# Performance work log

Measured on AMD Instinct MI355X. Metric: run time of the kernel, lower is better.

The kernel has to match this reference:

```python
import jax, jax.numpy as jnp
import numpy as np

B, L, D, H = 2, 2048, 1024, 16
DK = D // H
DFF = 4 * D
EPS = 1e-5  # torch LayerNorm default


def setup_inputs() -> dict:
    key = jax.random.key(0)
    ks = jax.random.split(key, 12)
    w = lambda k, shp: (jax.random.normal(k, shp, jnp.float32) * 0.02)
    return {
        "x": jax.random.normal(ks[0], (B, L, D), jnp.float32),
        "y": jax.random.normal(ks[1], (B, L, D), jnp.float32),
        "Wq": w(ks[2], (D, D)), "bq": jnp.zeros((D,), jnp.float32),
        "Wk": w(ks[3], (D, D)), "bk": jnp.zeros((D,), jnp.float32),
        "Wv": w(ks[4], (D, D)), "bv": jnp.zeros((D,), jnp.float32),
        "Wo": w(ks[5], (D, D)), "bo": jnp.zeros((D,), jnp.float32),
        "W1": w(ks[6], (D, DFF)), "b1": jnp.zeros((DFF,), jnp.float32),
        "W2": w(ks[7], (DFF, D)), "b2": jnp.zeros((D,), jnp.float32),
        "ln1_w": jnp.ones((L, D), jnp.float32), "ln1_b": jnp.zeros((L, D), jnp.float32),
        "ln2_w": jnp.ones((L, D), jnp.float32), "ln2_b": jnp.zeros((L, D), jnp.float32),
    }


def _layernorm2d(t, w, b):
    # nn.LayerNorm(normalized_shape=[L, D]): normalize jointly over last two dims
    mu = jnp.mean(t, axis=(-2, -1), keepdims=True)
    var = jnp.mean((t - mu) ** 2, axis=(-2, -1), keepdims=True)
    return (t - mu) * jax.lax.rsqrt(var + EPS) * w + b


def _attention(q_in, kv_in, Wq, bq, Wk, bk, Wv, bv, Wo, bo):
    split = lambda t: t.reshape(B, L, H, DK).transpose(0, 2, 1, 3)  # [B,H,L,DK]
    q = split(q_in @ Wq + bq)
    k = split(kv_in @ Wk + bk)
    v = split(kv_in @ Wv + bv)
    scores = jnp.einsum("bhqd,bhkd->bhqk", q, k) / (DK ** 0.5)
    # NOTE: original applies torch.tril to SCORES (zeroes upper triangle,
    # NOT -inf), so future positions still contribute exp(0)=1 in softmax.
    scores = jnp.tril(scores)
    p_attn = jax.nn.softmax(scores, axis=-1)
    out = jnp.einsum("bhqk,bhkd->bhqd", p_attn, v)
    out = out.transpose(0, 2, 1, 3).reshape(B, L, D)
    return out @ Wo + bo


def reference(x, y, Wq, bq, Wk, bk, Wv, bv, Wo, bo, W1, b1, W2, b2,
              ln1_w, ln1_b, ln2_w, ln2_b):
    # sublayer 0: pre-norm y, attention(query=x, key=value=norm(y)), residual
    y1 = y + _attention(x, _layernorm2d(y, ln1_w, ln1_b),
                        Wq, bq, Wk, bk, Wv, bv, Wo, bo)
    # sublayer 1: pre-norm, FFN (dropout inactive in eval), residual
    h = jax.nn.relu(_layernorm2d(y1, ln2_w, ln2_b) @ W1 + b1)
    return y1 + h @ W2 + b2
```

## Files before the change

kernel.cpp:

```cpp
#include <hip/hip_runtime.h>
#include <math.h>

#define B 2
#define L 2048
#define D 1024
#define H 16
#define DK 64
#define DFF 4096
#define EPS 1e-5f

typedef short short8 __attribute__((ext_vector_type(8)));
typedef short short4v __attribute__((ext_vector_type(4)));
typedef float float4v __attribute__((ext_vector_type(4)));
typedef unsigned int u32;

__device__ inline short f2bf(float f) {
    unsigned u = __builtin_bit_cast(unsigned, f);
    u += 0x7fffu + ((u >> 16) & 1u);
    return (short)(u >> 16);
}

__device__ inline float bf2f(short s) {
    unsigned u = ((unsigned)(unsigned short)s) << 16;
    return __builtin_bit_cast(float, u);
}

#define GLOAD_LDS16(gp, lp)                                                  \
    __builtin_amdgcn_global_load_lds(                                        \
        (const __attribute__((address_space(1))) u32*)(const void*)(gp),     \
        (__attribute__((address_space(3))) u32*)(void*)(lp), 16, 0, 0)

__device__ inline void xcd_remap(int& bx, int& by) {
    const int nbx = gridDim.x, nby = gridDim.y;
    const int orig = blockIdx.x + nbx * blockIdx.y;
    const int k = orig & 7, j = orig >> 3;
    const int nyc = nby >> 3;
    bx = j % nbx;
    by = k * nyc + j / nbx;
}


__global__ __launch_bounds__(256) void red_partial(const float* __restrict__ X,
                                                   float* __restrict__ part) {
    int b = blockIdx.y;
    const float4* p = (const float4*)(X + (size_t)b * L * D);
    float s = 0.f, ss = 0.f;
    for (int idx = blockIdx.x * 256 + threadIdx.x; idx < L * D / 4; idx += 256 * 256) {
        float4 v = p[idx];
        s += v.x + v.y + v.z + v.w;
        ss += v.x * v.x + v.y * v.y + v.z * v.z + v.w * v.w;
    }
    __shared__ float sh0[256], sh1[256];
    sh0[threadIdx.x] = s; sh1[threadIdx.x] = ss;
    __syncthreads();
    for (int o = 128; o; o >>= 1) {
        if (threadIdx.x < o) {
            sh0[threadIdx.x] += sh0[threadIdx.x + o];
            sh1[threadIdx.x] += sh1[threadIdx.x + o];
        }
        __syncthreads();
    }
    if (threadIdx.x == 0) {
        part[(b * 256 + blockIdx.x) * 2 + 0] = sh0[0];
        part[(b * 256 + blockIdx.x) * 2 + 1] = sh1[0];
    }
}

__global__ __launch_bounds__(256) void red_final(const float* __restrict__ part,
                                                 float* __restrict__ stats) {
    int b = blockIdx.x;
    float s = part[(b * 256 + threadIdx.x) * 2 + 0];
    float ss = part[(b * 256 + threadIdx.x) * 2 + 1];
    __shared__ float sh0[256], sh1[256];
    sh0[threadIdx.x] = s; sh1[threadIdx.x] = ss;
    __syncthreads();
    for (int o = 128; o; o >>= 1) {
        if (threadIdx.x < o) {
            sh0[threadIdx.x] += sh0[threadIdx.x + o];
            sh1[threadIdx.x] += sh1[threadIdx.x + o];
        }
        __syncthreads();
    }
    if (threadIdx.x == 0) {
        const float invN = 1.f / (float)(L * D);
        float mu = sh0[0] * invN;
        float var = sh1[0] * invN - mu * mu;
        stats[b * 2 + 0] = mu;
        stats[b * 2 + 1] = rsqrtf(var + EPS);
    }
}

__global__ __launch_bounds__(256) void ln_apply_bf(const float* __restrict__ X,
                                                   const float* __restrict__ W,
                                                   const float* __restrict__ Bb,
                                                   const float* __restrict__ stats,
                                                   short* __restrict__ Yn) {
    int b = blockIdx.y;
    float mu = stats[b * 2 + 0];
    float rstd = stats[b * 2 + 1];
    size_t e = (size_t)(blockIdx.x * 256 + threadIdx.x) * 4;
    const float4 xv = *(const float4*)(X + (size_t)b * L * D + e);
    const float4 wv = *(const float4*)(W + e);
    const float4 bv = *(const float4*)(Bb + e);
    short4v o;
    o[0] = f2bf((xv.x - mu) * rstd * wv.x + bv.x);
    o[1] = f2bf((xv.y - mu) * rstd * wv.y + bv.y);
    o[2] = f2bf((xv.z - mu) * rstd * wv.z + bv.z);
    o[3] = f2bf((xv.w - mu) * rstd * wv.w + bv.w);
    *(short4v*)(Yn + (size_t)b * L * D + e) = o;
}

__global__ __launch_bounds__(256) void convert_bf(const float* __restrict__ X,
                                                  short* __restrict__ Y) {
    size_t e = (size_t)(blockIdx.x * 256 + threadIdx.x) * 4;
    const float4 v = *(const float4*)(X + e);
    short4v o = {f2bf(v.x), f2bf(v.y), f2bf(v.z), f2bf(v.w)};
    *(short4v*)(Y + e) = o;
}

__global__ __launch_bounds__(256) void wt_transpose(const float* __restrict__ W,
                                                    short* __restrict__ WT,
                                                    int K, int N) {
    __shared__ short tile[32][33];
    const int t = threadIdx.x;
    const int tx = t & 31, ty = t >> 5;
    const int k0 = blockIdx.y * 32, n0 = blockIdx.x * 32;
#pragma unroll
    for (int i = 0; i < 4; ++i) {
        const int k = ty + i * 8;
        tile[k][tx] = f2bf(W[(size_t)(k0 + k) * N + n0 + tx]);
    }
    __syncthreads();
#pragma unroll
    for (int i = 0; i < 4; ++i) {
        const int n = ty + i * 8;
        WT[(size_t)(n0 + n) * K + k0 + tx] = tile[tx][n];
    }
}


__device__ __forceinline__ void cv128_body(const short* __restrict__ A,
                                           const short* __restrict__ BT,
                                           const float* __restrict__ bias,
                                           const float* __restrict__ Res,
                                           void* __restrict__ Cout,
                                           int N, int Kloop, int lda, int flags,
                                           int m0, int n0,
                                           short* __restrict__ AsB,
                                           short* __restrict__ BsB) {
    const int t = threadIdx.x;
    const int wave = t >> 6, lane = t & 63;
    const int m16 = lane & 15, q4 = lane >> 4;
    const int wm = (wave >> 1) * 64, wn = (wave & 1) * 64;
    const int xorm = m16 & 7;
    const int BUFE = 128 * 64;

    float4v acc[4][4];
#pragma unroll
    for (int i = 0; i < 4; ++i)
#pragma unroll
        for (int j = 0; j < 4; ++j) acc[i][j] = (float4v){0.f, 0.f, 0.f, 0.f};

    auto stage = [&](int buf, int k0) {
        short* AsBuf = AsB + buf * BUFE;
        short* BsBuf = BsB + buf * BUFE;
#pragma unroll
        for (int p = 0; p < 4; ++p) {
            const int s = p * 256 + t;
            const int row = s >> 3;
            const int col = ((s & 7) ^ (row & 7)) * 8;
            GLOAD_LDS16(A + (size_t)(m0 + row) * lda + k0 + col,
                        AsBuf + (p * 256 + wave * 64) * 8);
        }
#pragma unroll
        for (int p = 0; p < 4; ++p) {
            const int s = p * 256 + t;
            const int row = s >> 3;
            const int col = ((s & 7) ^ (row & 7)) * 8;
            GLOAD_LDS16(BT + (size_t)(n0 + row) * lda + k0 + col,
                        BsBuf + (p * 256 + wave * 64) * 8);
        }
    };

    auto compute = [&](int buf) {
        const short* AsBuf = AsB + buf * BUFE;
        const short* BsBuf = BsB + buf * BUFE;
#pragma unroll
        for (int kk = 0; kk < 2; ++kk) {
            const int slot = ((kk * 4 + q4) ^ xorm) * 8;
            short8 af[4], bf[4];
#pragma unroll
            for (int mi = 0; mi < 4; ++mi)
                af[mi] = *(const short8*)&AsBuf[(wm + mi * 16 + m16) * 64 + slot];
#pragma unroll
            for (int ni = 0; ni < 4; ++ni)
                bf[ni] = *(const short8*)&BsBuf[(wn + ni * 16 + m16) * 64 + slot];
#pragma unroll
            for (int mi = 0; mi < 4; ++mi)
#pragma unroll
                for (int ni = 0; ni < 4; ++ni)
                    acc[mi][ni] = __builtin_amdgcn_mfma_f32_16x16x32_bf16(
                        af[mi], bf[ni], acc[mi][ni], 0, 0, 0);
        }
    };

    const int nt = Kloop >> 6;
    stage(0, 0);
    for (int ti = 0; ti < nt; ++ti) {
        const int cur = ti & 1;
        if (ti + 1 < nt) {
            stage(cur ^ 1, (ti + 1) << 6);
            asm volatile("s_waitcnt vmcnt(8)" ::: "memory");
        } else {
            asm volatile("s_waitcnt vmcnt(0)" ::: "memory");
        }
        __builtin_amdgcn_s_barrier();
        __builtin_amdgcn_sched_barrier(0);
        compute(cur);
        __builtin_amdgcn_s_barrier();
    }

#pragma unroll
    for (int mi = 0; mi < 4; ++mi)
#pragma unroll
        for (int ni = 0; ni < 4; ++ni) {
            const int col = n0 + wn + ni * 16 + m16;
            const float bb = bias ? bias[col] : 0.f;
#pragma unroll
            for (int r = 0; r < 4; ++r) {
                const int row = m0 + wm + mi * 16 + q4 * 4 + r;
                float v = acc[mi][ni][r] + bb;
                if (Res) v += Res[(size_t)row * N + col];
                if (flags & 1) v = fmaxf(v, 0.f);
                if (flags & 2)
                    ((short*)Cout)[(size_t)row * N + col] = f2bf(v);
                else
                    ((float*)Cout)[(size_t)row * N + col] = v;
            }
        }
}

__global__ __launch_bounds__(256) void gemm_cv128(const short* __restrict__ A,
                                                  const short* __restrict__ BT,
                                                  const float* __restrict__ bias,
                                                  const float* __restrict__ Res,
                                                  void* __restrict__ Cout,
                                                  int M, int N, int K, int flags) {
    __shared__ short As[2][128 * 64];
    __shared__ short Bs[2][128 * 64];
    int bx, by;
    xcd_remap(bx, by);
    cv128_body(A, BT, bias, Res, Cout, N, K, K, flags, by * 128, bx * 128,
               &As[0][0], &Bs[0][0]);
}

__global__ __launch_bounds__(256) void gemm_qkv(const short* __restrict__ xb,
                                                const short* __restrict__ WqT,
                                                const float* __restrict__ bq,
                                                short* __restrict__ qb,
                                                const short* __restrict__ ynb,
                                                const short* __restrict__ WkvT,
                                                const float* __restrict__ bkv,
                                                short* __restrict__ kvb) {
    __shared__ short As[2][128 * 64];
    __shared__ short Bs[2][128 * 64];
    const int id = blockIdx.x;
    const int k = id & 7, j = id >> 3;
    const int lin = k * 96 + j;
    if (lin < 256) {
        const int bx = lin & 7, by = lin >> 3;
        cv128_body(xb, WqT, bq, nullptr, qb, 1024, 1024, 1024, 2,
                   by * 128, bx * 128, &As[0][0], &Bs[0][0]);
    } else {
        const int l2 = lin - 256;
        const int bx = l2 & 15, by = l2 >> 4;
        cv128_body(ynb, WkvT, bkv, nullptr, kvb, 2048, 1024, 1024, 2,
                   by * 128, bx * 128, &As[0][0], &Bs[0][0]);
    }
}

__global__ __launch_bounds__(256) void gemm_cv128_sk(const short* __restrict__ A,
                                                     const short* __restrict__ BT,
                                                     float* __restrict__ part,
                                                     int M, int N, int K) {
    __shared__ short As[2][128 * 64];
    __shared__ short Bs[2][128 * 64];
    const int id = blockIdx.x;
    const int k = id & 7, j = id >> 3;
    const int lin = k * 64 + j;
    const int ks = lin >> 8;
    const int rem = lin & 255;
    const int by = rem & 31, bx = (rem >> 5) & 7;
    const int Kc = K >> 1;
    cv128_body(A + ks * Kc, BT + ks * Kc, nullptr, nullptr,
               part + (size_t)ks * M * N, N, Kc, K, 0,
               by * 128, bx * 128, &As[0][0], &Bs[0][0]);
}

__global__ __launch_bounds__(256) void sk_reduce(const float* __restrict__ part,
                                                 const float* __restrict__ bias,
                                                 const float* __restrict__ Res,
                                                 float* __restrict__ out,
                                                 int MN, int N) {
    const size_t e = (size_t)(blockIdx.x * 256 + threadIdx.x) * 4;
    const float4 p0 = *(const float4*)(part + e);
    const float4 p1 = *(const float4*)(part + (size_t)MN + e);
    const float4 rv = *(const float4*)(Res + e);
    const float4 bv = *(const float4*)(bias + (e & (size_t)(N - 1)));
    float4 o;
    o.x = p0.x + p1.x + rv.x + bv.x;
    o.y = p0.y + p1.y + rv.y + bv.y;
    o.z = p0.z + p1.z + rv.z + bv.z;
    o.w = p0.w + p1.w + rv.w + bv.w;
    *(float4*)(out + e) = o;
}

__global__ __launch_bounds__(512) void gemm_cv256(const short* __restrict__ A,
                                                  const short* __restrict__ BT,
                                                  const float* __restrict__ bias,
                                                  const float* __restrict__ Res,
                                                  void* __restrict__ Cout,
                                                  int M, int N, int K, int flags) {
    __shared__ short As[2][256 * 64];
    __shared__ short Bs[2][256 * 64];
    const int t = threadIdx.x;
    const int wave = t >> 6, lane = t & 63;
    const int m16 = lane & 15, q4 = lane >> 4;
    int bx, by;
    xcd_remap(bx, by);
    const int m0 = by * 256, n0 = bx * 256;
    const int wm = (wave >> 2) * 128, wn = (wave & 3) * 64;
    const int xorm = m16 & 7;

    float4v acc[8][4];
#pragma unroll
    for (int i = 0; i < 8; ++i)
#pragma unroll
        for (int j = 0; j < 4; ++j) acc[i][j] = (float4v){0.f, 0.f, 0.f, 0.f};

    auto stage = [&](int buf, int k0) {
#pragma unroll
        for (int p = 0; p < 4; ++p) {
            const int s = p * 512 + t;
            const int row = s >> 3;
            const int col = ((s & 7) ^ (row & 7)) * 8;
            short* lds = &As[buf][(p * 512 + wave * 64) * 8];
            GLOAD_LDS16(A + (size_t)(m0 + row) * K + k0 + col, lds);
        }
#pragma unroll
        for (int p = 0; p < 4; ++p) {
            const int s = p * 512 + t;
            const int row = s >> 3;
            const int col = ((s & 7) ^ (row & 7)) * 8;
            short* lds = &Bs[buf][(p * 512 + wave * 64) * 8];
            GLOAD_LDS16(BT + (size_t)(n0 + row) * K + k0 + col, lds);
        }
    };

    auto compute = [&](int buf) {
#pragma unroll
        for (int kk = 0; kk < 2; ++kk) {
            const int slot = ((kk * 4 + q4) ^ xorm) * 8;
            short8 af[8], bf[4];
#pragma unroll
            for (int mi = 0; mi < 8; ++mi)
                af[mi] = *(const short8*)&As[buf][(wm + mi * 16 + m16) * 64 + slot];
#pragma unroll
            for (int ni = 0; ni < 4; ++ni)
                bf[ni] = *(const short8*)&Bs[buf][(wn + ni * 16 + m16) * 64 + slot];
#pragma unroll
            for (int mi = 0; mi < 8; ++mi)
#pragma unroll
                for (int ni = 0; ni < 4; ++ni)
                    acc[mi][ni] = __builtin_amdgcn_mfma_f32_16x16x32_bf16(
                        af[mi], bf[ni], acc[mi][ni], 0, 0, 0);
        }
    };

    const int nt = K >> 6;
    stage(0, 0);
    for (int ti = 0; ti < nt; ++ti) {
        const int cur = ti & 1;
        if (ti + 1 < nt) {
            stage(cur ^ 1, (ti + 1) << 6);
            asm volatile("s_waitcnt vmcnt(8)" ::: "memory");
        } else {
            asm volatile("s_waitcnt vmcnt(0)" ::: "memory");
        }
        __builtin_amdgcn_s_barrier();
        __builtin_amdgcn_sched_barrier(0);
        compute(cur);
        __builtin_amdgcn_s_barrier();
    }

#pragma unroll
    for (int mi = 0; mi < 8; ++mi)
#pragma unroll
        for (int ni = 0; ni < 4; ++ni) {
            const int col = n0 + wn + ni * 16 + m16;
            const float bb = bias[col];
#pragma unroll
            for (int r = 0; r < 4; ++r) {
                const int row = m0 + wm + mi * 16 + q4 * 4 + r;
                float v = acc[mi][ni][r] + bb;
                if (Res) v += Res[(size_t)row * N + col];
                if (flags & 1) v = fmaxf(v, 0.f);
                if (flags & 2)
                    ((short*)Cout)[(size_t)row * N + col] = f2bf(v);
                else
                    ((float*)Cout)[(size_t)row * N + col] = v;
            }
        }
}


#define ASTR 72
#define SKV (2 * D)

__global__ __launch_bounds__(256) void v_tilesum(const short* __restrict__ KVg,
                                                 float* __restrict__ Vtile) {
    const int bh = blockIdx.x >> 5;
    const int kt = blockIdx.x & 31;
    const int b = bh >> 4, h = bh & (H - 1);
    const size_t baseV = (size_t)b * L * SKV + (size_t)h * DK + D;
    const int d = threadIdx.x & 63, g = threadIdx.x >> 6;
    float s = 0.f;
    for (int j = g * 16; j < g * 16 + 16; ++j)
        s += bf2f(KVg[baseV + (size_t)(kt * 64 + j) * SKV + d]);
    __shared__ float sh[4][64];
    sh[g][d] = s;
    __syncthreads();
    if (threadIdx.x < 64)
        Vtile[((size_t)bh * 32 + kt) * 64 + d] = sh[0][d] + sh[1][d] + sh[2][d] + sh[3][d];
}

__global__ __launch_bounds__(64) void v_suffix(const float* __restrict__ Vtile,
                                               float* __restrict__ Vsuf) {
    const int bh = blockIdx.x;
    const int d = threadIdx.x;
    float s = 0.f;
    Vsuf[((size_t)bh * 33 + 32) * 64 + d] = 0.f;
    for (int kt = 31; kt >= 0; --kt) {
        s += Vtile[((size_t)bh * 32 + kt) * 64 + d];
        Vsuf[((size_t)bh * 33 + kt) * 64 + d] = s;
    }
}


__device__ inline void attn_stage_load(const short* __restrict__ KVg,
                                       size_t baseK, int kt0, int sj, int sd8,
                                       short8* kr, short8* vr) {
#pragma unroll
    for (int rep = 0; rep < 2; ++rep) {
        const int j = rep * 32 + sj;
        const size_t g = baseK + (size_t)(kt0 + j) * SKV + sd8;
        kr[rep] = *(const short8*)(KVg + g);
        vr[rep] = *(const short8*)(KVg + g + D);
    }
}

__device__ inline void attn_stage_write(short* __restrict__ KbB,
                                        short* __restrict__ VtB,
                                        int sj, int sd8,
                                        const short8* kr, const short8* vr) {
    const int sm = sd8 >> 3;
#pragma unroll
    for (int rep = 0; rep < 2; ++rep) {
        const int j = rep * 32 + sj;
        *(short8*)&KbB[j * ASTR + sd8] = kr[rep];
        const int jsw = ((((j >> 3) ^ sm) << 3) | (j & 7));
#pragma unroll
        for (int i = 0; i < 8; ++i) VtB[(sd8 + i) * ASTR + jsw] = vr[rep][i];
    }
}

__global__ __launch_bounds__(256) void attn_mfma(const short* __restrict__ Qg,
                                                 const short* __restrict__ KVg,
                                                 const float* __restrict__ Vsuf,
                                                 short* __restrict__ O) {
    __shared__ alignas(16) short Kb[2][64 * ASTR];
    __shared__ alignas(16) short Vt[2][64 * ASTR];
    __shared__ alignas(16) short Pb[64 * ASTR];

    const int t = threadIdx.x;
    const int wave = t >> 6;
    const int lane = t & 63;
    const int m16 = lane & 15;
    const int q4 = lane >> 4;

    const int u = blockIdx.x & 15;
    const int bh = blockIdx.x >> 4;
    const int h = bh & (H - 1);
    const int b = bh >> 4;
    const size_t baseQ = (size_t)b * L * D + (size_t)h * DK;
    const size_t baseK = (size_t)b * L * SKV + (size_t)h * DK;

    const int sj = t >> 3;
    const int sd8 = (t & 7) * 8;

    const int irow = wave * 16 + m16;
    const int ig = irow >> 3;

#pragma unroll
    for (int pq = 0; pq < 2; ++pq) {
        const int qt = pq ? (31 - u) : u;
        const int q0 = qt * 64;
        const int rowA = q0 + wave * 16 + m16;

        short8 qf[2];
#pragma unroll
        for (int kc = 0; kc < 2; ++kc)
            qf[kc] = *(const short8*)(Qg + baseQ + (size_t)rowA * D + kc * 32 + q4 * 8);

        float lsum = 0.f;
        float4v acc[4];
#pragma unroll
        for (int f = 0; f < 4; ++f) acc[f] = (float4v){0.f, 0.f, 0.f, 0.f};

        {
            short8 kr[2], vr[2];
            attn_stage_load(KVg, baseK, 0, sj, sd8, kr, vr);
            attn_stage_write(&Kb[0][0], &Vt[0][0], sj, sd8, kr, vr);
        }
        __syncthreads();

        for (int kt = 0; kt <= qt; ++kt) {
            const int cur = kt & 1;
            const short* KbC = &Kb[cur][0];
            const short* VtC = &Vt[cur][0];

            short8 kr[2], vr[2];
            if (kt < qt)
                attn_stage_load(KVg, baseK, (kt + 1) * 64, sj, sd8, kr, vr);

            const bool diag = (kt == qt);

#pragma unroll
            for (int f = 0; f < 4; ++f) {
                const short8 kf0 = *(const short8*)&KbC[(f * 16 + m16) * ASTR + q4 * 8];
                const short8 kf1 = *(const short8*)&KbC[(f * 16 + m16) * ASTR + 32 + q4 * 8];
                float4v sv = {0.f, 0.f, 0.f, 0.f};
                sv = __builtin_amdgcn_mfma_f32_16x16x32_bf16(kf0, qf[0], sv, 0, 0, 0);
                sv = __builtin_amdgcn_mfma_f32_16x16x32_bf16(kf1, qf[1], sv, 0, 0, 0);

                float pv[4];
                if (diag) {
#pragma unroll
                    for (int r = 0; r < 4; ++r) {
                        const int jl = f * 16 + q4 * 4 + r;
                        pv[r] = (jl <= irow) ? __expf(sv[r] * 0.125f) : 1.0f;
                    }
                } else {
#pragma unroll
                    for (int r = 0; r < 4; ++r) pv[r] = __expf(sv[r] * 0.125f);
                }
                lsum += pv[0] + pv[1] + pv[2] + pv[3];

                short4v s4;
                s4[0] = f2bf(pv[0]); s4[1] = f2bf(pv[1]);
                s4[2] = f2bf(pv[2]); s4[3] = f2bf(pv[3]);
                const int jb = f * 2 + (q4 >> 1);
                *(short4v*)&Pb[irow * ASTR + (((jb ^ ig) << 3) | ((q4 & 1) << 2))] = s4;
            }

#pragma unroll
            for (int kc = 0; kc < 2; ++kc) {
                const short8 pf = *(const short8*)&Pb[irow * ASTR + (((kc * 4 + q4) ^ ig) << 3)];
#pragma unroll
                for (int f = 0; f < 4; ++f) {
                    const int d = f * 16 + m16;
                    const short8 vf = *(const short8*)&VtC[d * ASTR + (((kc * 4 + q4) ^ (d >> 3)) << 3)];
                    acc[f] = __builtin_amdgcn_mfma_f32_16x16x32_bf16(pf, vf, acc[f], 0, 0, 0);
                }
            }

            if (kt < qt)
                attn_stage_write(&Kb[cur ^ 1][0], &Vt[cur ^ 1][0], sj, sd8, kr, vr);
            __syncthreads();
        }

        float s = lsum;
        s += __shfl_xor(s, 16);
        s += __shfl_xor(s, 32);
        s += (float)(L - (qt + 1) * 64);
        const float inv = 1.0f / s;
        float invr[4];
#pragma unroll
        for (int r = 0; r < 4; ++r) invr[r] = __shfl(inv, q4 * 4 + r);

        const float* vs = Vsuf + ((size_t)bh * 33 + qt + 1) * 64;
#pragma unroll
        for (int f = 0; f < 4; ++f) {
            const float vadd = vs[f * 16 + m16];
#pragma unroll
            for (int r = 0; r < 4; ++r) {
                const int i = q0 + wave * 16 + q4 * 4 + r;
                O[baseQ + (size_t)i * D + f * 16 + m16] = f2bf((acc[f][r] + vadd) * invr[r]);
            }
        }
    }
}


extern "C" void kernel_launch(void* const* d_in, const int* in_sizes, int n_in,
                              void* d_out, int out_size, void* d_ws, size_t ws_size,
                              hipStream_t stream) {
    const float* x    = (const float*)d_in[0];
    const float* y    = (const float*)d_in[1];
    const float* Wq   = (const float*)d_in[2];
    const float* bq   = (const float*)d_in[3];
    const float* Wk   = (const float*)d_in[4];
    const float* bk   = (const float*)d_in[5];
    const float* Wv   = (const float*)d_in[6];
    const float* bv   = (const float*)d_in[7];
    const float* Wo   = (const float*)d_in[8];
    const float* bo   = (const float*)d_in[9];
    const float* W1   = (const float*)d_in[10];
    const float* b1   = (const float*)d_in[11];
    const float* W2   = (const float*)d_in[12];
    const float* b2   = (const float*)d_in[13];
    const float* ln1w = (const float*)d_in[14];
    const float* ln1b = (const float*)d_in[15];
    const float* ln2w = (const float*)d_in[16];
    const float* ln2b = (const float*)d_in[17];
    float* out = (float*)d_out;

    const size_t F = (size_t)B * L * D;
    char* p = (char*)d_ws;
    short* xb    = (short*)p; p += F * 2;
    short* ynb   = (short*)p; p += F * 2;
    short* qb    = (short*)p; p += F * 2;
    short* kvb   = (short*)p; p += 2 * F * 2;
    short* aob   = (short*)p; p += F * 2;
    short* y1nb  = (short*)p; p += F * 2;
    short* hb    = (short*)p; p += (size_t)B * L * DFF * 2;
    float* y1    = (float*)p; p += F * 4;
    short* WqT   = (short*)p; p += (size_t)D * D * 2;
    short* WkvT  = (short*)p; p += (size_t)D * 2 * D * 2;
    short* WoT   = (short*)p; p += (size_t)D * D * 2;
    short* W1T   = (short*)p; p += (size_t)D * DFF * 2;
    short* W2T   = (short*)p; p += (size_t)D * DFF * 2;
    float* biaskv= (float*)p; p += 2 * D * 4;
    float* vtile = (float*)p; p += (size_t)B * H * 32 * DK * 4;
    float* vsuf  = (float*)p; p += (size_t)B * H * 33 * DK * 4;
    float* part  = (float*)p; p += B * 256 * 2 * 4;
    float* stats = (float*)p;

    float* skpart = (float*)qb;

    const int M = B * L;

    wt_transpose<<<dim3(D / 32, D / 32), 256, 0, stream>>>(Wq, WqT, D, D);
    wt_transpose<<<dim3(D / 32, D / 32), 256, 0, stream>>>(Wk, WkvT, D, D);
    wt_transpose<<<dim3(D / 32, D / 32), 256, 0, stream>>>(Wv, WkvT + (size_t)D * D, D, D);
    wt_transpose<<<dim3(D / 32, D / 32), 256, 0, stream>>>(Wo, WoT, D, D);
    wt_transpose<<<dim3(DFF / 32, D / 32), 256, 0, stream>>>(W1, W1T, D, DFF);
    wt_transpose<<<dim3(D / 32, DFF / 32), 256, 0, stream>>>(W2, W2T, DFF, D);
    hipMemcpyAsync(biaskv,     bk, D * sizeof(float), hipMemcpyDeviceToDevice, stream);
    hipMemcpyAsync(biaskv + D, bv, D * sizeof(float), hipMemcpyDeviceToDevice, stream);

    convert_bf<<<dim3(F / 1024), 256, 0, stream>>>(x, xb);

    red_partial<<<dim3(256, B), 256, 0, stream>>>(y, part);
    red_final<<<dim3(B), 256, 0, stream>>>(part, stats);
    ln_apply_bf<<<dim3(L * D / 1024, B), 256, 0, stream>>>(y, ln1w, ln1b, stats, ynb);

    gemm_qkv<<<dim3(768), 256, 0, stream>>>(xb, WqT, bq, qb, ynb, WkvT, biaskv, kvb);

    v_tilesum<<<dim3(B * H * 32), 256, 0, stream>>>(kvb, vtile);
    v_suffix<<<dim3(B * H), 64, 0, stream>>>(vtile, vsuf);

    attn_mfma<<<dim3(B * H * 16), 256, 0, stream>>>(qb, kvb, vsuf, aob);

    gemm_cv128<<<dim3(D / 128, M / 128), 256, 0, stream>>>(aob, WoT, bo, y, y1, M, D, D, 0);

    red_partial<<<dim3(256, B), 256, 0, stream>>>(y1, part);
    red_final<<<dim3(B), 256, 0, stream>>>(part, stats);
    ln_apply_bf<<<dim3(L * D / 1024, B), 256, 0, stream>>>(y1, ln2w, ln2b, stats, y1nb);

    gemm_cv256<<<dim3(DFF / 256, M / 256), 512, 0, stream>>>(y1nb, W1T, b1, nullptr, hb, M, DFF, D, 3);

    gemm_cv128_sk<<<dim3(512), 256, 0, stream>>>(hb, W2T, skpart, M, D, DFF);
    sk_reduce<<<dim3(M * D / 1024), 256, 0, stream>>>(skpart, b2, y1, out, M * D, D);
}
```

Baseline: 427.3 us.

## Pre-transpose V globally and stage K/V tiles via direct global-to-LDS loads

Adds a v_transpose kernel that writes V in [bh, d, L] layout into the unused FFN hidden buffer. The attention kernel then stages K and transposed V tiles with async global-to-LDS loads into XOR-swizzled unpadded tiles, using vmcnt waits and raw barriers in place of register staging and scalar LDS transposes. This removes per-tile register round-trips and scattered 2-byte LDS writes from the attention loop. The cost is an extra launch plus V transpose traffic, and it depends on the GLOAD_LDS16 macro and on getting waitcnt and barrier ordering right.

```diff
diff --git a/kernel.cpp b/kernel.cpp
--- a/kernel.cpp
+++ b/kernel.cpp
@@ -447,39 +447,42 @@
 }
 
 
-__device__ inline void attn_stage_load(const short* __restrict__ KVg,
-                                       size_t baseK, int kt0, int sj, int sd8,
-                                       short8* kr, short8* vr) {
+__global__ __launch_bounds__(256) void v_transpose(const short* __restrict__ KVg,
+                                                   short* __restrict__ VT) {
+    __shared__ short tile[64 * ASTR];
+    const int t = threadIdx.x;
+    const int bh = blockIdx.x >> 5;
+    const int jt = blockIdx.x & 31;
+    const int b = bh >> 4, h = bh & (H - 1);
+    const size_t baseV = (size_t)b * L * SKV + (size_t)h * DK + D;
+    const int j0 = jt * 64;
+    const int sj = t >> 3, sd8 = (t & 7) * 8, sm = t & 7;
 #pragma unroll
     for (int rep = 0; rep < 2; ++rep) {
         const int j = rep * 32 + sj;
-        const size_t g = baseK + (size_t)(kt0 + j) * SKV + sd8;
-        kr[rep] = *(const short8*)(KVg + g);
-        vr[rep] = *(const short8*)(KVg + g + D);
-    }
-}
-
-__device__ inline void attn_stage_write(short* __restrict__ KbB,
-                                        short* __restrict__ VtB,
-                                        int sj, int sd8,
-                                        const short8* kr, const short8* vr) {
-    const int sm = sd8 >> 3;
+        const short8 vv = *(const short8*)(KVg + baseV + (size_t)(j0 + j) * SKV + sd8);
+        const int jsw = ((((j >> 3) ^ sm) << 3) | (j & 7));
+#pragma unroll
+        for (int i = 0; i < 8; ++i) tile[(sd8 + i) * ASTR + jsw] = vv[i];
+    }
+    __syncthreads();
 #pragma unroll
     for (int rep = 0; rep < 2; ++rep) {
-        const int j = rep * 32 + sj;
-        *(short8*)&KbB[j * ASTR + sd8] = kr[rep];
-        const int jsw = ((((j >> 3) ^ sm) << 3) | (j & 7));
-#pragma unroll
-        for (int i = 0; i < 8; ++i) VtB[(sd8 + i) * ASTR + jsw] = vr[rep][i];
-    }
-}
+        const int s = rep * 256 + t;
+        const int d = s >> 3, c = s & 7;
+        const short8 vv = *(const short8*)&tile[d * ASTR + ((c ^ (d >> 3)) << 3)];
+        *(short8*)(VT + ((size_t)bh * DK + d) * L + j0 + c * 8) = vv;
+    }
+}
+
 
 __global__ __launch_bounds__(256) void attn_mfma(const short* __restrict__ Qg,
                                                  const short* __restrict__ KVg,
+                                                 const short* __restrict__ VTg,
                                                  const float* __restrict__ Vsuf,
                                                  short* __restrict__ O) {
-    __shared__ alignas(16) short Kb[2][64 * ASTR];
-    __shared__ alignas(16) short Vt[2][64 * ASTR];
+    __shared__ alignas(16) short Kb[2][64 * 64];
+    __shared__ alignas(16) short Vt[2][64 * 64];
     __shared__ alignas(16) short Pb[64 * ASTR];
 
     const int t = threadIdx.x;
@@ -494,12 +497,30 @@
     const int b = bh >> 4;
     const size_t baseQ = (size_t)b * L * D + (size_t)h * DK;
     const size_t baseK = (size_t)b * L * SKV + (size_t)h * DK;
-
-    const int sj = t >> 3;
-    const int sd8 = (t & 7) * 8;
+    const size_t baseVT = (size_t)bh * DK * L;
 
     const int irow = wave * 16 + m16;
     const int ig = irow >> 3;
+    const int xorm = m16 & 7;
+
+    auto stage = [&](int buf, int kt0) {
+#pragma unroll
+        for (int rep = 0; rep < 2; ++rep) {
+            const int s = rep * 256 + t;
+            const int j = s >> 3;
+            const int c = (s & 7) ^ (j & 7);
+            GLOAD_LDS16(KVg + baseK + (size_t)(kt0 + j) * SKV + c * 8,
+                        &Kb[buf][(rep * 256 + wave * 64) * 8]);
+        }
+#pragma unroll
+        for (int rep = 0; rep < 2; ++rep) {
+            const int s = rep * 256 + t;
+            const int d = s >> 3;
+            const int c = (s & 7) ^ (d & 7);
+            GLOAD_LDS16(VTg + baseVT + (size_t)d * L + kt0 + c * 8,
+                        &Vt[buf][(rep * 256 + wave * 64) * 8]);
+        }
+    };
 
 #pragma unroll
     for (int pq = 0; pq < 2; ++pq) {
@@ -517,28 +538,27 @@
 #pragma unroll
         for (int f = 0; f < 4; ++f) acc[f] = (float4v){0.f, 0.f, 0.f, 0.f};
 
-        {
-            short8 kr[2], vr[2];
-            attn_stage_load(KVg, baseK, 0, sj, sd8, kr, vr);
-            attn_stage_write(&Kb[0][0], &Vt[0][0], sj, sd8, kr, vr);
-        }
-        __syncthreads();
-
+        stage(0, 0);
         for (int kt = 0; kt <= qt; ++kt) {
             const int cur = kt & 1;
+            if (kt < qt) {
+                stage(cur ^ 1, (kt + 1) * 64);
+                asm volatile("s_waitcnt vmcnt(4)" ::: "memory");
+            } else {
+                asm volatile("s_waitcnt vmcnt(0)" ::: "memory");
+            }
+            __builtin_amdgcn_s_barrier();
+            __builtin_amdgcn_sched_barrier(0);
+
             const short* KbC = &Kb[cur][0];
             const short* VtC = &Vt[cur][0];
-
-            short8 kr[2], vr[2];
-            if (kt < qt)
-                attn_stage_load(KVg, baseK, (kt + 1) * 64, sj, sd8, kr, vr);
-
             const bool diag = (kt == qt);
 
 #pragma unroll
             for (int f = 0; f < 4; ++f) {
-                const short8 kf0 = *(const short8*)&KbC[(f * 16 + m16) * ASTR + q4 * 8];
-                const short8 kf1 = *(const short8*)&KbC[(f * 16 + m16) * ASTR + 32 + q4 * 8];
+                const int krow = f * 16 + m16;
+                const short8 kf0 = *(const short8*)&KbC[krow * 64 + ((q4 ^ xorm) << 3)];
+                const short8 kf1 = *(const short8*)&KbC[krow * 64 + (((4 + q4) ^ xorm) << 3)];
                 float4v sv = {0.f, 0.f, 0.f, 0.f};
                 sv = __builtin_amdgcn_mfma_f32_16x16x32_bf16(kf0, qf[0], sv, 0, 0, 0);
                 sv = __builtin_amdgcn_mfma_f32_16x16x32_bf16(kf1, qf[1], sv, 0, 0, 0);
@@ -569,14 +589,11 @@
 #pragma unroll
                 for (int f = 0; f < 4; ++f) {
                     const int d = f * 16 + m16;
-                    const short8 vf = *(const short8*)&VtC[d * ASTR + (((kc * 4 + q4) ^ (d >> 3)) << 3)];
+                    const short8 vf = *(const short8*)&VtC[d * 64 + (((kc * 4 + q4) ^ xorm) << 3)];
                     acc[f] = __builtin_amdgcn_mfma_f32_16x16x32_bf16(pf, vf, acc[f], 0, 0, 0);
                 }
             }
-
-            if (kt < qt)
-                attn_stage_write(&Kb[cur ^ 1][0], &Vt[cur ^ 1][0], sj, sd8, kr, vr);
-            __syncthreads();
+            __builtin_amdgcn_s_barrier();
         }
 
         float s = lsum;
@@ -646,6 +663,7 @@
     float* part  = (float*)p; p += B * 256 * 2 * 4;
     float* stats = (float*)p;
 
+    short* vtb = hb;
     float* skpart = (float*)qb;
 
     const int M = B * L;
@@ -667,10 +685,11 @@
 
     gemm_qkv<<<dim3(768), 256, 0, stream>>>(xb, WqT, bq, qb, ynb, WkvT, biaskv, kvb);
 
+    v_transpose<<<dim3(B * H * 32), 256, 0, stream>>>(kvb, vtb);
     v_tilesum<<<dim3(B * H * 32), 256, 0, stream>>>(kvb, vtile);
     v_suffix<<<dim3(B * H), 64, 0, stream>>>(vtile, vsuf);
 
-    attn_mfma<<<dim3(B * H * 16), 256, 0, stream>>>(qb, kvb, vsuf, aob);
+    attn_mfma<<<dim3(B * H * 16), 256, 0, stream>>>(qb, kvb, vtb, vsuf, aob);
 
     gemm_cv128<<<dim3(D / 128, M / 128), 256, 0, stream>>>(aob, WoT, bo, y, y1, M, D, D, 0);
 
```

New measurement: 429.3 us. Within noise of the previous version (+0.5%).
